# Performance work log

Measured on AMD Instinct MI355X. Metric: run time of the kernel, lower is better.

The kernel has to match this reference:

```python
import jax, jax.numpy as jnp
import numpy as np
from jax import lax

N = 128          # number of SDE time steps (== len(grad_u))
T_FINAL = 1.0    # t
D = 0.5          # diffusion coefficient
DT = T_FINAL / N
RB = 1.05        # assumed reflecting-sphere boundary radius for xb
B = 65536        # batch
H = 64           # FNN hidden width
SQRT2D = float(np.sqrt(2.0 * D))
# grad_eucl_polar buffer from the module
G_EP = jnp.array([[0.0, 0.0], [0.0, 1.0], [-1.0, 0.0]], dtype=jnp.float32)


def fnn(x, W0, b0, W1, b1, W2, b2):
    # utils.FNN(in,out,64,3): 3-layer tanh MLP
    h = jnp.tanh(x @ W0 + b0)
    h = jnp.tanh(h @ W1 + b1)
    return h @ W2 + b2


def t_inverse(a, phi):
    # T_inverse([theta - pi/2, phi]) = Rz(phi) @ Ry(a); maps fix_x=[1,0,0] to xt.
    ca, sa = jnp.cos(a), jnp.sin(a)
    cp, sp = jnp.cos(phi), jnp.sin(phi)
    z = jnp.zeros_like(a)
    r0 = jnp.stack([cp * ca, -sp, cp * sa], axis=-1)
    r1 = jnp.stack([sp * ca, cp, sp * sa], axis=-1)
    r2 = jnp.stack([-sa, z, ca], axis=-1)
    return jnp.stack([r0, r1, r2], axis=1)  # [B,3,3]


def _forward(xt0, dBt, W0u, b0u, W1u, b1u, W2u, b2u, Wg0, bg0, Wg1, bg1, Wg2, bg2):
    u_pre0 = fnn(xt0, W0u, b0u, W1u, b1u, W2u, b2u)  # u(x0), [B,1]
    eye = jnp.broadcast_to(jnp.eye(3, dtype=xt0.dtype), (xt0.shape[0], 3, 3))

    def step(carry, inp):
        xt, xt_in, gt, u_pre = carry
        dB, w0, c0, w1, c1, w2, c2 = inp
        # polar_corr(xt) with theta shifted by pi/2
        r = jnp.linalg.norm(xt, axis=1)
        theta = jnp.arccos(jnp.clip(xt[:, 2] / r, -0.999999, 0.999999))
        phi = jnp.arctan2(xt[:, 1], xt[:, 0])
        Ti = t_inverse(theta - jnp.pi / 2, phi)  # [B,3,3]
        # grad_u term: (g^T @ grad_trans @ T_inv)^T * grad_eucl_polar, summed over dim 1
        g = fnn(xt_in, w0, c0, w1, c1, w2, c2)  # [B,3]
        v = jnp.einsum('bi,bij,bjk->bk', g, gt, Ti)  # [B,3]
        gu = v @ G_EP  # [B,2]
        u_pre = u_pre + SQRT2D * jnp.sum(gu * dB, axis=1, keepdims=True)
        # sde_sphere step
        d = SQRT2D * dB
        td = d[:, 0] + jnp.pi / 2
        pd = d[:, 1]
        # transform_x(dXt) - fix_x  (spherical -> Cartesian, minus pole)
        dX3 = jnp.stack([jnp.sin(td) * jnp.cos(pd) - 1.0,
                         jnp.sin(td) * jnp.sin(pd),
                         jnp.cos(td)], axis=1)  # [B,3]
        dX = jnp.einsum('bij,bj->bi', Ti, dX3)
        xt = xt + dX
        xi = xt_in + jnp.einsum('bij,bj->bi', gt, dX)
        # go_back: reflect across sphere of radius RB where outside
        ri = jnp.linalg.norm(xi, axis=1)
        n = xi / ri[:, None]  # outward normal nb
        out = ri > RB
        xt_in = jnp.where(out[:, None], xi - 2.0 * (ri - RB)[:, None] * n, xi)
        # grad_trans += (-2 n n^T) grad_trans  where reflected (Householder)
        m = jnp.einsum('bj,bjk->bk', n, gt)
        gt = jnp.where(out[:, None, None], gt - 2.0 * n[:, :, None] * m[:, None, :], gt)
        return (xt, xt_in, gt, u_pre), None

    (xt, xt_in, gt, u_pre), _ = lax.scan(step, (xt0, xt0, eye, u_pre0),
                                         (dBt, Wg0, bg0, Wg1, bg1, Wg2, bg2))
    u_rel = jnp.sum(xt_in ** 2, axis=1, keepdims=True)  # assumed u0 terminal condition
    return u_pre, u_rel


def setup_inputs() -> dict:
    key = jax.random.key(0)
    ks = jax.random.split(key, 8)
    xt0 = jax.random.normal(ks[0], (B, 3), jnp.float32)
    xt0 = xt0 / jnp.linalg.norm(xt0, axis=1, keepdims=True)  # data_gen: points on unit sphere
    dBt = jax.random.normal(ks[1], (N, B, 2), jnp.float32) * np.float32(np.sqrt(DT))

    def w(k, shape, fan_in):
        return jax.random.normal(k, shape, jnp.float32) / np.float32(np.sqrt(fan_in))

    return {
        'xt0': xt0, 'dBt': dBt,
        'W0u': w(ks[2], (3, H), 3), 'b0u': jnp.zeros((H,), jnp.float32),
        'W1u': w(ks[3], (H, H), H), 'b1u': jnp.zeros((H,), jnp.float32),
        'W2u': w(ks[4], (H, 1), H), 'b2u': jnp.zeros((1,), jnp.float32),
        'Wg0': w(ks[5], (N, 3, H), 3), 'bg0': jnp.zeros((N, H), jnp.float32),
        'Wg1': w(ks[6], (N, H, H), H), 'bg1': jnp.zeros((N, H), jnp.float32),
        'Wg2': w(ks[7], (N, H, 3), H), 'bg2': jnp.zeros((N, 3), jnp.float32),
    }


def reference(xt0, dBt, W0u, b0u, W1u, b1u, W2u, b2u, Wg0, bg0, Wg1, bg1, Wg2, bg2):
    return _forward(xt0, dBt, W0u, b0u, W1u, b1u, W2u, b2u, Wg0, bg0, Wg1, bg1, Wg2, bg2)
```

## Files before the change

### kernel.cpp

```cpp
#include <hip/hip_runtime.h>

#define NB 65536
#define NSTEP 128
#define HD 64
#define RB 1.05f
#define SCALE 2.8853900817779268f
#define TBLK 928
#define OFF_A1 0
#define OFF_A0 512
#define OFF_A2 768
#define OFF_CB 896

typedef __bf16 bf16x8 __attribute__((ext_vector_type(8)));
typedef float f32x4 __attribute__((ext_vector_type(4)));
typedef unsigned int uint;
typedef unsigned short ushort;

extern "C" __device__ float __ocml_native_exp2_f32(float);
#if __has_builtin(__builtin_amdgcn_exp2f)
#define EXP2(x) __builtin_amdgcn_exp2f(x)
#else
#define EXP2(x) __ocml_native_exp2_f32(x)
#endif

__device__ __forceinline__ float tanh_fast(float x) {
    float e2 = __expf(2.0f * x);
    return 1.0f - 2.0f * __builtin_amdgcn_rcpf(1.0f + e2);
}

__device__ __forceinline__ void tanh2s(float za, float zb, float& ta, float& tb) {
    float ea = EXP2(za);
    float eb = EXP2(zb);
    float a1 = 1.0f + ea;
    float b1 = 1.0f + eb;
    float rp = __builtin_amdgcn_rcpf(a1 * b1);
    ta = fmaf(-2.0f * b1, rp, 1.0f);
    tb = fmaf(-2.0f * a1, rp, 1.0f);
}

__device__ __forceinline__ void sincos_small(float x, float& s, float& c) {
    float x2 = x * x;
    s = fmaf(x2, fmaf(x2, 8.3333333e-3f, -0.16666667f), 1.0f) * x;
    c = fmaf(x2, fmaf(x2, fmaf(x2, -1.3888889e-3f, 4.1666668e-2f), -0.5f), 1.0f);
}

__device__ __forceinline__ uint pack_bf16_trunc(float a, float b) {
    return __builtin_amdgcn_perm(__float_as_uint(b), __float_as_uint(a), 0x07060302u);
}

__device__ __forceinline__ ushort bf16_rne(float f) {
    uint u = __float_as_uint(f);
    u += 0x7fffu + ((u >> 16) & 1u);
    return (ushort)(u >> 16);
}


__global__ __launch_bounds__(256) void prep_a1(const float* __restrict__ Wg1,
                                               uint4* __restrict__ wsB) {
    int tid  = blockIdx.x * 256 + threadIdx.x;
    int lane = tid & 63;
    int I    = (tid >> 6) & 3;
    int kk   = (tid >> 8) & 1;
    int t    = tid >> 9;
    int rA   = lane & 15;
    int lrow = (I & 1) * 4 + (I >> 1) * 32 + (rA >> 2) * 8 + (rA & 3);
    int k0   = kk * 32 + ((lane >> 4) & 3) * 8;
    const float* src = Wg1 + ((size_t)t * HD + k0) * HD + lrow;
    ushort o[8];
#pragma unroll
    for (int e = 0; e < 8; e++) o[e] = bf16_rne(src[(size_t)e * HD] * SCALE);
    uint4 v;
    v.x = (uint)o[0] | ((uint)o[1] << 16);
    v.y = (uint)o[2] | ((uint)o[3] << 16);
    v.z = (uint)o[4] | ((uint)o[5] << 16);
    v.w = (uint)o[6] | ((uint)o[7] << 16);
    wsB[(size_t)t * TBLK + OFF_A1 + (kk * 4 + I) * 64 + lane] = v;
}

__global__ __launch_bounds__(256) void prep_a0(const float* __restrict__ Wg0,
                                               const float* __restrict__ bg0,
                                               uint4* __restrict__ wsB) {
    int tid  = blockIdx.x * 256 + threadIdx.x;
    int lane = tid & 63;
    int I    = (tid >> 6) & 3;
    int t    = tid >> 8;
    int m    = lane & 15;
    int kg   = (lane >> 4) & 3;
    int h    = (I >> 1) * 32 + (m >> 2) * 8 + (I & 1) * 4 + (m & 3);
    ushort o[8];
#pragma unroll
    for (int e = 0; e < 8; e++) {
        int k = kg * 8 + e;
        float v;
        if (k < 3)       v = SCALE * Wg0[((size_t)t * 3 + k) * HD + h];
        else if (k == 3) v = SCALE * bg0[(size_t)t * HD + h];
        else             v = 0.0f;
        o[e] = bf16_rne(v);
    }
    uint4 v;
    v.x = (uint)o[0] | ((uint)o[1] << 16);
    v.y = (uint)o[2] | ((uint)o[3] << 16);
    v.z = (uint)o[4] | ((uint)o[5] << 16);
    v.w = (uint)o[6] | ((uint)o[7] << 16);
    wsB[(size_t)t * TBLK + OFF_A0 + I * 64 + lane] = v;
}

__global__ __launch_bounds__(256) void prep_a2(const float* __restrict__ Wg2,
                                               uint4* __restrict__ wsB) {
    int tid  = blockIdx.x * 256 + threadIdx.x;
    int lane = tid & 63;
    int kk   = (tid >> 6) & 1;
    int t    = tid >> 7;
    int row  = lane & 15;
    int k0   = kk * 32 + ((lane >> 4) & 3) * 8;
    ushort o[8];
#pragma unroll
    for (int e = 0; e < 8; e++) {
        float v = (row < 3) ? Wg2[(size_t)t * HD * 3 + (size_t)(k0 + e) * 3 + row] : 0.0f;
        o[e] = bf16_rne(v);
    }
    uint4 v;
    v.x = (uint)o[0] | ((uint)o[1] << 16);
    v.y = (uint)o[2] | ((uint)o[3] << 16);
    v.z = (uint)o[4] | ((uint)o[5] << 16);
    v.w = (uint)o[6] | ((uint)o[7] << 16);
    wsB[(size_t)t * TBLK + OFF_A2 + kk * 64 + lane] = v;
}

__global__ __launch_bounds__(256) void prep_bias(const float* __restrict__ bg1,
                                                 uint4* __restrict__ wsB) {
    int tid = blockIdx.x * 256 + threadIdx.x;
    int i   = tid & 127;
    int t   = tid >> 7;
    int r   = i & 63;
    int pi  = ((r >> 4) & 1) * 4 + ((r >> 5) & 1) * 32 + ((r >> 2) & 3) * 8 + (r & 3);
    float* dst = (float*)(wsB + (size_t)t * TBLK + OFF_CB);
    dst[i] = (i < 64) ? (SCALE * bg1[(size_t)t * HD + pi]) : 0.0f;
}

__device__ __forceinline__ void mlp_h2_unpacked(float xx, float xy, float xz,
                                                const float* __restrict__ w0,
                                                const float* __restrict__ c0,
                                                const float* __restrict__ w1,
                                                int lane, f32x4* acc) {
    const int g16 = (lane >> 4) & 3;
    const int l15 = lane & 15;
#pragma unroll
    for (int kk = 0; kk < 2; kk++) {
        bf16x8 af[4];
#pragma unroll
        for (int I = 0; I < 4; I++) {
            uint pk[4];
#pragma unroll
            for (int ep = 0; ep < 4; ep++) {
                float f0 = w1[(kk * 32 + g16 * 8 + 2 * ep + 0) * HD + I * 16 + l15];
                float f1 = w1[(kk * 32 + g16 * 8 + 2 * ep + 1) * HD + I * 16 + l15];
                pk[ep] = (uint)bf16_rne(f0) | ((uint)bf16_rne(f1) << 16);
            }
            uint4 v; v.x = pk[0]; v.y = pk[1]; v.z = pk[2]; v.w = pk[3];
            af[I] = __builtin_bit_cast(bf16x8, v);
        }
        const float* wk = w0 + kk * 32 + g16 * 8;
        float4 wxa = *(const float4*)(wk);
        float4 wxb = *(const float4*)(wk + 4);
        float4 wya = *(const float4*)(wk + HD);
        float4 wyb = *(const float4*)(wk + HD + 4);
        float4 wza = *(const float4*)(wk + 2 * HD);
        float4 wzb = *(const float4*)(wk + 2 * HD + 4);
        const float* ck = c0 + kk * 32 + g16 * 8;
        float4 cva = *(const float4*)(ck);
        float4 cvb = *(const float4*)(ck + 4);
        float p0 = fmaf(xx, wxa.x, fmaf(xy, wya.x, fmaf(xz, wza.x, cva.x)));
        float p1 = fmaf(xx, wxa.y, fmaf(xy, wya.y, fmaf(xz, wza.y, cva.y)));
        float p2 = fmaf(xx, wxa.z, fmaf(xy, wya.z, fmaf(xz, wza.z, cva.z)));
        float p3 = fmaf(xx, wxa.w, fmaf(xy, wya.w, fmaf(xz, wza.w, cva.w)));
        float p4 = fmaf(xx, wxb.x, fmaf(xy, wyb.x, fmaf(xz, wzb.x, cvb.x)));
        float p5 = fmaf(xx, wxb.y, fmaf(xy, wyb.y, fmaf(xz, wzb.y, cvb.y)));
        float p6 = fmaf(xx, wxb.z, fmaf(xy, wyb.z, fmaf(xz, wzb.z, cvb.z)));
        float p7 = fmaf(xx, wxb.w, fmaf(xy, wyb.w, fmaf(xz, wzb.w, cvb.w)));
        uint4 bv;
        bv.x = pack_bf16_trunc(tanh_fast(p0), tanh_fast(p1));
        bv.y = pack_bf16_trunc(tanh_fast(p2), tanh_fast(p3));
        bv.z = pack_bf16_trunc(tanh_fast(p4), tanh_fast(p5));
        bv.w = pack_bf16_trunc(tanh_fast(p6), tanh_fast(p7));
        bf16x8 bf = __builtin_bit_cast(bf16x8, bv);
#pragma unroll
        for (int I = 0; I < 4; I++)
            acc[I] = __builtin_amdgcn_mfma_f32_16x16x32_bf16(af[I], bf, acc[I], 0, 0, 0);
    }
}

__global__ __launch_bounds__(256, 4) void sde_fast(
    const float* __restrict__ xt0,
    const float* __restrict__ dBt,
    const float* __restrict__ W0u, const float* __restrict__ b0u,
    const float* __restrict__ W1u, const float* __restrict__ b1u,
    const float* __restrict__ W2u, const float* __restrict__ b2u,
    const float* __restrict__ bg2,
    const uint4* __restrict__ wsB,
    float* __restrict__ out)
{
    const int tid  = threadIdx.x;
    const int lane = tid & 63;
    const int wv   = tid >> 6;
    const int g16  = (lane >> 4) & 3;
    const int l15  = lane & 15;
    const int p    = blockIdx.x * 64 + wv * 16 + l15;

    float xtx = xt0[p * 3 + 0];
    float xty = xt0[p * 3 + 1];
    float xtz = xt0[p * 3 + 2];
    float xix = xtx, xiy = xty, xiz = xtz;
    float g00 = 1.f, g01 = 0.f, g02 = 0.f;
    float g10 = 0.f, g11 = 1.f, g12 = 0.f;
    float g20 = 0.f, g21 = 0.f, g22 = 1.f;

    float u_pre;
    {
        f32x4 acc[4];
#pragma unroll
        for (int I = 0; I < 4; I++) acc[I] = (f32x4){0.f, 0.f, 0.f, 0.f};
        mlp_h2_unpacked(xtx, xty, xtz, W0u, b0u, W1u, lane, acc);
        float pj = 0.f;
#pragma unroll
        for (int I = 0; I < 4; I++) {
            float4 wv2 = *(const float4*)(W2u + I * 16 + g16 * 4);
            float4 cv  = *(const float4*)(b1u + I * 16 + g16 * 4);
            pj = fmaf(tanh_fast(acc[I][0] + cv.x), wv2.x, pj);
            pj = fmaf(tanh_fast(acc[I][1] + cv.y), wv2.y, pj);
            pj = fmaf(tanh_fast(acc[I][2] + cv.z), wv2.z, pj);
            pj = fmaf(tanh_fast(acc[I][3] + cv.w), wv2.w, pj);
        }
        pj += __shfl_xor(pj, 16, 64);
        pj += __shfl_xor(pj, 32, 64);
        u_pre = pj + b2u[0];
    }

    const f32x4 zero4 = (f32x4){0.f, 0.f, 0.f, 0.f};

#pragma unroll 1
    for (int t = 0; t < NSTEP; t++) {
        const uint4* blob_t = wsB + (size_t)t * TBLK;
        const float* c1p_t  = (const float*)(blob_t + OFF_CB);
        const float* c2     = bg2 + (size_t)t * 3;

        float d  = fmaf(xtx, xtx, fmaf(xty, xty, xtz * xtz));
        float rs = __builtin_amdgcn_rsqf(d);
        float uu = xtz * rs;
        uu = fminf(fmaxf(uu, -0.999999f), 0.999999f);
        float sa = -uu;
        float rho2 = fmaf(xtx, xtx, xty * xty);
        bool hasrho = rho2 > 0.0f;
        float rr = __builtin_amdgcn_rsqf(rho2);
        float cp = hasrho ? (xtx * rr) : 1.0f;
        float sp = hasrho ? (xty * rr) : 0.0f;
        float ca = hasrho ? (rho2 * rr * rs) : 1.4142135e-3f;
        float T00 = cp * ca, T01 = -sp, T02 = cp * sa;
        float T10 = sp * ca, T11 = cp,  T12 = sp * sa;
        float T20 = -sa,               T22 = ca;

        uint4 b0v;
        b0v.x = pack_bf16_trunc(xix, xiy);
        b0v.y = pack_bf16_trunc(xiz, 1.0f);
        b0v.z = 0u; b0v.w = 0u;
        bf16x8 b0 = __builtin_bit_cast(bf16x8, b0v);
        f32x4 acc0[4];
#pragma unroll
        for (int I = 0; I < 4; I++) {
            bf16x8 a0 = __builtin_bit_cast(bf16x8, blob_t[OFF_A0 + I * 64 + lane]);
            acc0[I] = __builtin_amdgcn_mfma_f32_16x16x32_bf16(a0, b0, zero4, 0, 0, 0);
        }

        f32x4 acc[4];
#pragma unroll
        for (int I = 0; I < 4; I++) {
            float4 cv = *(const float4*)(c1p_t + I * 16 + g16 * 4);
            acc[I] = (f32x4){cv.x, cv.y, cv.z, cv.w};
        }
#pragma unroll
        for (int kk = 0; kk < 2; kk++) {
            float t0, t1, t2, t3, t4, t5, t6, t7;
            tanh2s(acc0[kk * 2 + 0][0], acc0[kk * 2 + 0][1], t0, t1);
            tanh2s(acc0[kk * 2 + 0][2], acc0[kk * 2 + 0][3], t2, t3);
            tanh2s(acc0[kk * 2 + 1][0], acc0[kk * 2 + 1][1], t4, t5);
            tanh2s(acc0[kk * 2 + 1][2], acc0[kk * 2 + 1][3], t6, t7);
            uint4 bv;
            bv.x = pack_bf16_trunc(t0, t1);
            bv.y = pack_bf16_trunc(t2, t3);
            bv.z = pack_bf16_trunc(t4, t5);
            bv.w = pack_bf16_trunc(t6, t7);
            bf16x8 bf = __builtin_bit_cast(bf16x8, bv);
#pragma unroll
            for (int I = 0; I < 4; I++) {
                bf16x8 af = __builtin_bit_cast(bf16x8, blob_t[OFF_A1 + (kk * 4 + I) * 64 + lane]);
                acc[I] = __builtin_amdgcn_mfma_f32_16x16x32_bf16(af, bf, acc[I], 0, 0, 0);
            }
        }

        f32x4 acc2 = zero4;
#pragma unroll
        for (int half = 0; half < 2; half++) {
            float t0, t1, t2, t3, t4, t5, t6, t7;
            tanh2s(acc[2 * half + 0][0], acc[2 * half + 0][1], t0, t1);
            tanh2s(acc[2 * half + 0][2], acc[2 * half + 0][3], t2, t3);
            tanh2s(acc[2 * half + 1][0], acc[2 * half + 1][1], t4, t5);
            tanh2s(acc[2 * half + 1][2], acc[2 * half + 1][3], t6, t7);
            uint4 bv;
            bv.x = pack_bf16_trunc(t0, t1);
            bv.y = pack_bf16_trunc(t2, t3);
            bv.z = pack_bf16_trunc(t4, t5);
            bv.w = pack_bf16_trunc(t6, t7);
            bf16x8 bf = __builtin_bit_cast(bf16x8, bv);
            bf16x8 a2 = __builtin_bit_cast(bf16x8, blob_t[OFF_A2 + half * 64 + lane]);
            acc2 = __builtin_amdgcn_mfma_f32_16x16x32_bf16(a2, bf, acc2, 0, 0, 0);
        }
        float gv0 = __shfl(acc2[0], l15, 64) + c2[0];
        float gv1 = __shfl(acc2[1], l15, 64) + c2[1];
        float gv2 = __shfl(acc2[2], l15, 64) + c2[2];

        float M01 = fmaf(-sp, g00, cp * g01);
        float M11 = fmaf(-sp, g10, cp * g11);
        float M21 = fmaf(-sp, g20, cp * g21);
        float M02 = fmaf(g00, T02, fmaf(g01, T12, g02 * T22));
        float M12 = fmaf(g10, T02, fmaf(g11, T12, g12 * T22));
        float M22 = fmaf(g20, T02, fmaf(g21, T12, g22 * T22));
        float v1 = fmaf(gv0, M01, fmaf(gv1, M11, gv2 * M21));
        float v2 = fmaf(gv0, M02, fmaf(gv1, M12, gv2 * M22));

        const float2 dB = *(const float2*)(dBt + ((size_t)t * NB + p) * 2);
        float dB0 = dB.x, dB1 = dB.y;
        u_pre += fmaf(v1, dB1, -v2 * dB0);

        float s0d, c0d, s1d, c1d;
        sincos_small(dB0, s0d, c0d);
        sincos_small(dB1, s1d, c1d);
        float dx30 = fmaf(c0d, c1d, -1.0f);
        float dx31 = c0d * s1d;
        float dx32 = -s0d;

        float dX0 = fmaf(T00, dx30, fmaf(T01, dx31, T02 * dx32));
        float dX1 = fmaf(T10, dx30, fmaf(T11, dx31, T12 * dx32));
        float dX2 = fmaf(T20, dx30, T22 * dx32);

        xtx += dX0; xty += dX1; xtz += dX2;

        float xi0 = xix + fmaf(g00, dX0, fmaf(g01, dX1, g02 * dX2));
        float xi1 = xiy + fmaf(g10, dX0, fmaf(g11, dX1, g12 * dX2));
        float xi2 = xiz + fmaf(g20, dX0, fmaf(g21, dX1, g22 * dX2));

        float ri2 = fmaf(xi0, xi0, fmaf(xi1, xi1, xi2 * xi2));
        float rs2 = __builtin_amdgcn_rsqf(ri2);
        float ri  = ri2 * rs2;
        bool outb = ri > RB;
        float n0 = xi0 * rs2, n1 = xi1 * rs2, n2 = xi2 * rs2;
        float coefs = outb ? (2.0f * (ri - RB)) : 0.0f;

        xix = fmaf(-coefs, n0, xi0);
        xiy = fmaf(-coefs, n1, xi1);
        xiz = fmaf(-coefs, n2, xi2);

        float mm0 = fmaf(n0, g00, fmaf(n1, g10, n2 * g20));
        float mm1 = fmaf(n0, g01, fmaf(n1, g11, n2 * g21));
        float mm2 = fmaf(n0, g02, fmaf(n1, g12, n2 * g22));
        float tw  = outb ? 2.0f : 0.0f;
        float tn0 = tw * n0, tn1 = tw * n1, tn2 = tw * n2;
        g00 = fmaf(-tn0, mm0, g00);
        g01 = fmaf(-tn0, mm1, g01);
        g02 = fmaf(-tn0, mm2, g02);
        g10 = fmaf(-tn1, mm0, g10);
        g11 = fmaf(-tn1, mm1, g11);
        g12 = fmaf(-tn1, mm2, g12);
        g20 = fmaf(-tn2, mm0, g20);
        g21 = fmaf(-tn2, mm1, g21);
        g22 = fmaf(-tn2, mm2, g22);
    }

    float u_rel = fmaf(xix, xix, fmaf(xiy, xiy, xiz * xiz));
    if (g16 == 0) {
        out[p] = u_pre;
        out[NB + p] = u_rel;
    }
}

__global__ __launch_bounds__(256, 4) void sde_ref(
    const float* __restrict__ xt0,
    const float* __restrict__ dBt,
    const float* __restrict__ W0u, const float* __restrict__ b0u,
    const float* __restrict__ W1u, const float* __restrict__ b1u,
    const float* __restrict__ W2u, const float* __restrict__ b2u,
    const float* __restrict__ Wg0, const float* __restrict__ bg0,
    const float* __restrict__ Wg1, const float* __restrict__ bg1,
    const float* __restrict__ Wg2, const float* __restrict__ bg2,
    float* __restrict__ out)
{
    const int tid  = threadIdx.x;
    const int lane = tid & 63;
    const int wv   = tid >> 6;
    const int g16  = (lane >> 4) & 3;
    const int l15  = lane & 15;
    const int p    = blockIdx.x * 64 + wv * 16 + l15;

    float xtx = xt0[p * 3 + 0];
    float xty = xt0[p * 3 + 1];
    float xtz = xt0[p * 3 + 2];
    float xix = xtx, xiy = xty, xiz = xtz;
    float g00 = 1.f, g01 = 0.f, g02 = 0.f;
    float g10 = 0.f, g11 = 1.f, g12 = 0.f;
    float g20 = 0.f, g21 = 0.f, g22 = 1.f;

    float u_pre;
    {
        f32x4 acc[4];
#pragma unroll
        for (int I = 0; I < 4; I++) acc[I] = (f32x4){0.f, 0.f, 0.f, 0.f};
        mlp_h2_unpacked(xtx, xty, xtz, W0u, b0u, W1u, lane, acc);
        float pj = 0.f;
#pragma unroll
        for (int I = 0; I < 4; I++) {
            float4 wv2 = *(const float4*)(W2u + I * 16 + g16 * 4);
            float4 cv  = *(const float4*)(b1u + I * 16 + g16 * 4);
            pj = fmaf(tanh_fast(acc[I][0] + cv.x), wv2.x, pj);
            pj = fmaf(tanh_fast(acc[I][1] + cv.y), wv2.y, pj);
            pj = fmaf(tanh_fast(acc[I][2] + cv.z), wv2.z, pj);
            pj = fmaf(tanh_fast(acc[I][3] + cv.w), wv2.w, pj);
        }
        pj += __shfl_xor(pj, 16, 64);
        pj += __shfl_xor(pj, 32, 64);
        u_pre = pj + b2u[0];
    }

#pragma unroll 1
    for (int t = 0; t < NSTEP; t++) {
        const float* w0 = Wg0 + (size_t)t * 3 * HD;
        const float* c0 = bg0 + (size_t)t * HD;
        const float* c1 = bg1 + (size_t)t * HD;
        const float* w2 = Wg2 + (size_t)t * HD * 3;
        const float* c2 = bg2 + (size_t)t * 3;

        float r = sqrtf(fmaf(xtx, xtx, fmaf(xty, xty, xtz * xtz)));
        float uu = xtz / r;
        uu = fminf(fmaxf(uu, -0.999999f), 0.999999f);
        float ca = sqrtf((1.0f - uu) * (1.0f + uu));
        float sa = -uu;
        float rho = sqrtf(fmaf(xtx, xtx, xty * xty));
        float cp = (rho > 0.0f) ? (xtx / rho) : 1.0f;
        float sp = (rho > 0.0f) ? (xty / rho) : 0.0f;
        float T00 = cp * ca, T01 = -sp, T02 = cp * sa;
        float T10 = sp * ca, T11 = cp,  T12 = sp * sa;
        float T20 = -sa,               T22 = ca;

        f32x4 acc[4];
#pragma unroll
        for (int I = 0; I < 4; I++) acc[I] = (f32x4){0.f, 0.f, 0.f, 0.f};
        mlp_h2_unpacked(xix, xiy, xiz, w0, c0, Wg1 + (size_t)t * HD * HD, lane, acc);

        float pj0 = 0.f, pj1 = 0.f, pj2 = 0.f;
#pragma unroll
        for (int I = 0; I < 4; I++) {
            const float* wp = w2 + 3 * (I * 16 + g16 * 4);
            float4 wa = *(const float4*)(wp);
            float4 wb = *(const float4*)(wp + 4);
            float4 wc = *(const float4*)(wp + 8);
            float4 cv = *(const float4*)(c1 + I * 16 + g16 * 4);
            float th0 = tanh_fast(acc[I][0] + cv.x);
            float th1 = tanh_fast(acc[I][1] + cv.y);
            float th2 = tanh_fast(acc[I][2] + cv.z);
            float th3 = tanh_fast(acc[I][3] + cv.w);
            pj0 = fmaf(th0, wa.x, pj0); pj1 = fmaf(th0, wa.y, pj1); pj2 = fmaf(th0, wa.z, pj2);
            pj0 = fmaf(th1, wa.w, pj0); pj1 = fmaf(th1, wb.x, pj1); pj2 = fmaf(th1, wb.y, pj2);
            pj0 = fmaf(th2, wb.z, pj0); pj1 = fmaf(th2, wb.w, pj1); pj2 = fmaf(th2, wc.x, pj2);
            pj0 = fmaf(th3, wc.y, pj0); pj1 = fmaf(th3, wc.z, pj1); pj2 = fmaf(th3, wc.w, pj2);
        }
        pj0 += __shfl_xor(pj0, 16, 64); pj0 += __shfl_xor(pj0, 32, 64);
        pj1 += __shfl_xor(pj1, 16, 64); pj1 += __shfl_xor(pj1, 32, 64);
        pj2 += __shfl_xor(pj2, 16, 64); pj2 += __shfl_xor(pj2, 32, 64);
        float gv0 = pj0 + c2[0];
        float gv1 = pj1 + c2[1];
        float gv2 = pj2 + c2[2];

        float M01 = fmaf(-sp, g00, cp * g01);
        float M11 = fmaf(-sp, g10, cp * g11);
        float M21 = fmaf(-sp, g20, cp * g21);
        float M02 = fmaf(g00, T02, fmaf(g01, T12, g02 * T22));
        float M12 = fmaf(g10, T02, fmaf(g11, T12, g12 * T22));
        float M22 = fmaf(g20, T02, fmaf(g21, T12, g22 * T22));
        float v1 = fmaf(gv0, M01, fmaf(gv1, M11, gv2 * M21));
        float v2 = fmaf(gv0, M02, fmaf(gv1, M12, gv2 * M22));

        const float2 dB = *(const float2*)(dBt + ((size_t)t * NB + p) * 2);
        float dB0 = dB.x, dB1 = dB.y;
        u_pre += fmaf(v1, dB1, -v2 * dB0);

        float s0d, c0d, s1d, c1d;
        __sincosf(dB0, &s0d, &c0d);
        __sincosf(dB1, &s1d, &c1d);
        float dx30 = fmaf(c0d, c1d, -1.0f);
        float dx31 = c0d * s1d;
        float dx32 = -s0d;

        float dX0 = fmaf(T00, dx30, fmaf(T01, dx31, T02 * dx32));
        float dX1 = fmaf(T10, dx30, fmaf(T11, dx31, T12 * dx32));
        float dX2 = fmaf(T20, dx30, T22 * dx32);

        xtx += dX0; xty += dX1; xtz += dX2;

        float xi0 = xix + fmaf(g00, dX0, fmaf(g01, dX1, g02 * dX2));
        float xi1 = xiy + fmaf(g10, dX0, fmaf(g11, dX1, g12 * dX2));
        float xi2 = xiz + fmaf(g20, dX0, fmaf(g21, dX1, g22 * dX2));

        float ri = sqrtf(fmaf(xi0, xi0, fmaf(xi1, xi1, xi2 * xi2)));
        bool outb = ri > RB;
        float n0 = xi0 / ri, n1 = xi1 / ri, n2 = xi2 / ri;
        float coef = 2.0f * (ri - RB);

        xix = outb ? fmaf(-coef, n0, xi0) : xi0;
        xiy = outb ? fmaf(-coef, n1, xi1) : xi1;
        xiz = outb ? fmaf(-coef, n2, xi2) : xi2;

        float mm0 = fmaf(n0, g00, fmaf(n1, g10, n2 * g20));
        float mm1 = fmaf(n0, g01, fmaf(n1, g11, n2 * g21));
        float mm2 = fmaf(n0, g02, fmaf(n1, g12, n2 * g22));
        float tn0 = 2.0f * n0, tn1 = 2.0f * n1, tn2 = 2.0f * n2;
        g00 = outb ? fmaf(-tn0, mm0, g00) : g00;
        g01 = outb ? fmaf(-tn0, mm1, g01) : g01;
        g02 = outb ? fmaf(-tn0, mm2, g02) : g02;
        g10 = outb ? fmaf(-tn1, mm0, g10) : g10;
        g11 = outb ? fmaf(-tn1, mm1, g11) : g11;
        g12 = outb ? fmaf(-tn1, mm2, g12) : g12;
        g20 = outb ? fmaf(-tn2, mm0, g20) : g20;
        g21 = outb ? fmaf(-tn2, mm1, g21) : g21;
        g22 = outb ? fmaf(-tn2, mm2, g22) : g22;
    }

    float u_rel = fmaf(xix, xix, fmaf(xiy, xiy, xiz * xiz));
    if (g16 == 0) {
        out[p] = u_pre;
        out[NB + p] = u_rel;
    }
}

extern "C" void kernel_launch(void* const* d_in, const int* in_sizes, int n_in,
                              void* d_out, int out_size, void* d_ws, size_t ws_size,
                              hipStream_t stream) {
    const float* xt0 = (const float*)d_in[0];
    const float* dBt = (const float*)d_in[1];
    const float* W0u = (const float*)d_in[2];
    const float* b0u = (const float*)d_in[3];
    const float* W1u = (const float*)d_in[4];
    const float* b1u = (const float*)d_in[5];
    const float* W2u = (const float*)d_in[6];
    const float* b2u = (const float*)d_in[7];
    const float* Wg0 = (const float*)d_in[8];
    const float* bg0 = (const float*)d_in[9];
    const float* Wg1 = (const float*)d_in[10];
    const float* bg1 = (const float*)d_in[11];
    const float* Wg2 = (const float*)d_in[12];
    const float* bg2 = (const float*)d_in[13];
    float* out = (float*)d_out;

    const size_t needed = (size_t)NSTEP * TBLK * sizeof(uint4);
    dim3 grid(NB * 4 / 256), block(256);
    if (ws_size >= needed && d_ws != nullptr) {
        uint4* wsB = (uint4*)d_ws;
        hipLaunchKernelGGL(prep_a1,  dim3(256), dim3(256), 0, stream, Wg1, wsB);
        hipLaunchKernelGGL(prep_a0,  dim3(128), dim3(256), 0, stream, Wg0, bg0, wsB);
        hipLaunchKernelGGL(prep_a2,  dim3(64),  dim3(256), 0, stream, Wg2, wsB);
        hipLaunchKernelGGL(prep_bias, dim3(64), dim3(256), 0, stream, bg1, wsB);
        hipLaunchKernelGGL(sde_fast, grid, block, 0, stream,
                           xt0, dBt, W0u, b0u, W1u, b1u, W2u, b2u,
                           bg2, (const uint4*)wsB, out);
    } else {
        hipLaunchKernelGGL(sde_ref, grid, block, 0, stream,
                           xt0, dBt, W0u, b0u, W1u, b1u, W2u, b2u,
                           Wg0, bg0, Wg1, bg1, Wg2, bg2, out);
    }
}
```

Before: 415.9 us.

## Split SDE into state pass and time-parallel MLP pass with reduction

```diff
diff --git a/kernel.cpp b/kernel.cpp
--- a/kernel.cpp
+++ b/kernel.cpp
@@ -56,16 +56,19 @@
 
 
 __global__ __launch_bounds__(256) void prep_a1(const float* __restrict__ Wg1,
+                                               const float* __restrict__ W1u,
                                                uint4* __restrict__ wsB) {
     int tid  = blockIdx.x * 256 + threadIdx.x;
     int lane = tid & 63;
     int I    = (tid >> 6) & 3;
     int kk   = (tid >> 8) & 1;
     int t    = tid >> 9;
+    if (t > NSTEP) return;
     int rA   = lane & 15;
     int lrow = (I & 1) * 4 + (I >> 1) * 32 + (rA >> 2) * 8 + (rA & 3);
     int k0   = kk * 32 + ((lane >> 4) & 3) * 8;
-    const float* src = Wg1 + ((size_t)t * HD + k0) * HD + lrow;
+    const float* base = (t < NSTEP) ? (Wg1 + (size_t)t * HD * HD) : W1u;
+    const float* src  = base + (size_t)k0 * HD + lrow;
     ushort o[8];
 #pragma unroll
     for (int e = 0; e < 8; e++) o[e] = bf16_rne(src[(size_t)e * HD] * SCALE);
@@ -79,11 +82,14 @@
 
 __global__ __launch_bounds__(256) void prep_a0(const float* __restrict__ Wg0,
                                                const float* __restrict__ bg0,
+                                               const float* __restrict__ W0u,
+                                               const float* __restrict__ b0u,
                                                uint4* __restrict__ wsB) {
     int tid  = blockIdx.x * 256 + threadIdx.x;
     int lane = tid & 63;
     int I    = (tid >> 6) & 3;
     int t    = tid >> 8;
+    if (t > NSTEP) return;
     int m    = lane & 15;
     int kg   = (lane >> 4) & 3;
     int h    = (I >> 1) * 32 + (m >> 2) * 8 + (I & 1) * 4 + (m & 3);
@@ -91,10 +97,10 @@
 #pragma unroll
     for (int e = 0; e < 8; e++) {
         int k = kg * 8 + e;
-        float v;
-        if (k < 3)       v = SCALE * Wg0[((size_t)t * 3 + k) * HD + h];
-        else if (k == 3) v = SCALE * bg0[(size_t)t * HD + h];
-        else             v = 0.0f;
+        float v = 0.0f;
+        if (k < 3)       v = SCALE * ((t < NSTEP) ? Wg0[((size_t)t * 3 + k) * HD + h]
+                                                  : W0u[(size_t)k * HD + h]);
+        else if (k == 3) v = SCALE * ((t < NSTEP) ? bg0[(size_t)t * HD + h] : b0u[h]);
         o[e] = bf16_rne(v);
     }
     uint4 v;
@@ -106,17 +112,24 @@
 }
 
 __global__ __launch_bounds__(256) void prep_a2(const float* __restrict__ Wg2,
+                                               const float* __restrict__ W2u,
                                                uint4* __restrict__ wsB) {
     int tid  = blockIdx.x * 256 + threadIdx.x;
     int lane = tid & 63;
     int kk   = (tid >> 6) & 1;
     int t    = tid >> 7;
+    if (t > NSTEP) return;
     int row  = lane & 15;
+    int j    = row & 3;
     int k0   = kk * 32 + ((lane >> 4) & 3) * 8;
     ushort o[8];
 #pragma unroll
     for (int e = 0; e < 8; e++) {
-        float v = (row < 3) ? Wg2[(size_t)t * HD * 3 + (size_t)(k0 + e) * 3 + row] : 0.0f;
+        float v = 0.0f;
+        if (j < 3) {
+            if (t < NSTEP) v = Wg2[(size_t)t * HD * 3 + (size_t)(k0 + e) * 3 + j];
+            else           v = (j == 0) ? W2u[k0 + e] : 0.0f;
+        }
         o[e] = bf16_rne(v);
     }
     uint4 v;
@@ -128,14 +141,234 @@
 }
 
 __global__ __launch_bounds__(256) void prep_bias(const float* __restrict__ bg1,
+                                                 const float* __restrict__ b1u,
                                                  uint4* __restrict__ wsB) {
     int tid = blockIdx.x * 256 + threadIdx.x;
     int i   = tid & 127;
     int t   = tid >> 7;
+    if (t > NSTEP) return;
     int r   = i & 63;
     int pi  = ((r >> 4) & 1) * 4 + ((r >> 5) & 1) * 32 + ((r >> 2) & 3) * 8 + (r & 3);
     float* dst = (float*)(wsB + (size_t)t * TBLK + OFF_CB);
-    dst[i] = (i < 64) ? (SCALE * bg1[(size_t)t * HD + pi]) : 0.0f;
+    float v = 0.0f;
+    if (i < 64) v = SCALE * ((t < NSTEP) ? bg1[(size_t)t * HD + pi] : b1u[pi]);
+    dst[i] = v;
+}
+
+__device__ __forceinline__ f32x4 mlp_chain(float xx, float xy, float xz,
+                                           const uint4* __restrict__ blob_t,
+                                           int lane, int g16) {
+    const f32x4 zero4 = (f32x4){0.f, 0.f, 0.f, 0.f};
+    uint4 b0v;
+    b0v.x = pack_bf16_trunc(xx, xy);
+    b0v.y = pack_bf16_trunc(xz, 1.0f);
+    b0v.z = 0u; b0v.w = 0u;
+    bf16x8 b0 = __builtin_bit_cast(bf16x8, b0v);
+
+    uint4 a0v0 = {0u,0u,0u,0u}, a0v1 = {0u,0u,0u,0u}, a0v2 = {0u,0u,0u,0u}, a0v3 = {0u,0u,0u,0u};
+    if (g16 == 0) {
+        a0v0 = blob_t[OFF_A0 + 0 * 64 + lane];
+        a0v1 = blob_t[OFF_A0 + 1 * 64 + lane];
+        a0v2 = blob_t[OFF_A0 + 2 * 64 + lane];
+        a0v3 = blob_t[OFF_A0 + 3 * 64 + lane];
+    }
+    f32x4 acc0[4];
+    acc0[0] = __builtin_amdgcn_mfma_f32_16x16x32_bf16(__builtin_bit_cast(bf16x8, a0v0), b0, zero4, 0, 0, 0);
+    acc0[1] = __builtin_amdgcn_mfma_f32_16x16x32_bf16(__builtin_bit_cast(bf16x8, a0v1), b0, zero4, 0, 0, 0);
+    acc0[2] = __builtin_amdgcn_mfma_f32_16x16x32_bf16(__builtin_bit_cast(bf16x8, a0v2), b0, zero4, 0, 0, 0);
+    acc0[3] = __builtin_amdgcn_mfma_f32_16x16x32_bf16(__builtin_bit_cast(bf16x8, a0v3), b0, zero4, 0, 0, 0);
+
+    const float* c1p_t = (const float*)(blob_t + OFF_CB);
+    f32x4 acc[4];
+#pragma unroll
+    for (int I = 0; I < 4; I++) {
+        float4 cv = *(const float4*)(c1p_t + I * 16 + g16 * 4);
+        acc[I] = (f32x4){cv.x, cv.y, cv.z, cv.w};
+    }
+#pragma unroll
+    for (int kk = 0; kk < 2; kk++) {
+        float t0, t1, t2, t3, t4, t5, t6, t7;
+        tanh2s(acc0[kk * 2 + 0][0], acc0[kk * 2 + 0][1], t0, t1);
+        tanh2s(acc0[kk * 2 + 0][2], acc0[kk * 2 + 0][3], t2, t3);
+        tanh2s(acc0[kk * 2 + 1][0], acc0[kk * 2 + 1][1], t4, t5);
+        tanh2s(acc0[kk * 2 + 1][2], acc0[kk * 2 + 1][3], t6, t7);
+        uint4 bv;
+        bv.x = pack_bf16_trunc(t0, t1);
+        bv.y = pack_bf16_trunc(t2, t3);
+        bv.z = pack_bf16_trunc(t4, t5);
+        bv.w = pack_bf16_trunc(t6, t7);
+        bf16x8 bf = __builtin_bit_cast(bf16x8, bv);
+#pragma unroll
+        for (int I = 0; I < 4; I++) {
+            bf16x8 af = __builtin_bit_cast(bf16x8, blob_t[OFF_A1 + (kk * 4 + I) * 64 + lane]);
+            acc[I] = __builtin_amdgcn_mfma_f32_16x16x32_bf16(af, bf, acc[I], 0, 0, 0);
+        }
+    }
+    f32x4 acc2 = zero4;
+#pragma unroll
+    for (int half = 0; half < 2; half++) {
+        float t0, t1, t2, t3, t4, t5, t6, t7;
+        tanh2s(acc[2 * half + 0][0], acc[2 * half + 0][1], t0, t1);
+        tanh2s(acc[2 * half + 0][2], acc[2 * half + 0][3], t2, t3);
+        tanh2s(acc[2 * half + 1][0], acc[2 * half + 1][1], t4, t5);
+        tanh2s(acc[2 * half + 1][2], acc[2 * half + 1][3], t6, t7);
+        uint4 bv;
+        bv.x = pack_bf16_trunc(t0, t1);
+        bv.y = pack_bf16_trunc(t2, t3);
+        bv.z = pack_bf16_trunc(t4, t5);
+        bv.w = pack_bf16_trunc(t6, t7);
+        bf16x8 bf = __builtin_bit_cast(bf16x8, bv);
+        bf16x8 a2 = __builtin_bit_cast(bf16x8, blob_t[OFF_A2 + half * 64 + lane]);
+        acc2 = __builtin_amdgcn_mfma_f32_16x16x32_bf16(a2, bf, acc2, 0, 0, 0);
+    }
+    return acc2;
+}
+
+__global__ __launch_bounds__(256) void sde_state(
+    const float* __restrict__ xt0, const float* __restrict__ dBt,
+    float4* __restrict__ xiw4, float2* __restrict__ w2f,
+    float* __restrict__ out)
+{
+    int p = blockIdx.x * 256 + threadIdx.x;
+    float xtx = xt0[p * 3 + 0];
+    float xty = xt0[p * 3 + 1];
+    float xtz = xt0[p * 3 + 2];
+    float xix = xtx, xiy = xty, xiz = xtz;
+    float g00 = 1.f, g01 = 0.f, g02 = 0.f;
+    float g10 = 0.f, g11 = 1.f, g12 = 0.f;
+    float g20 = 0.f, g21 = 0.f, g22 = 1.f;
+
+    float2 dBa = *(const float2*)(dBt + (size_t)p * 2);
+    float2 dBb = *(const float2*)(dBt + ((size_t)NB + p) * 2);
+
+#pragma unroll 1
+    for (int t = 0; t < NSTEP; t++) {
+        float d  = fmaf(xtx, xtx, fmaf(xty, xty, xtz * xtz));
+        float rs = __builtin_amdgcn_rsqf(d);
+        float uu = xtz * rs;
+        uu = fminf(fmaxf(uu, -0.999999f), 0.999999f);
+        float sa = -uu;
+        float rho2 = fmaf(xtx, xtx, xty * xty);
+        bool hasrho = rho2 > 0.0f;
+        float rr = __builtin_amdgcn_rsqf(rho2);
+        float cp = hasrho ? (xtx * rr) : 1.0f;
+        float sp = hasrho ? (xty * rr) : 0.0f;
+        float ca = hasrho ? (rho2 * rr * rs) : 1.4142135e-3f;
+        float T00 = cp * ca, T01 = -sp, T02 = cp * sa;
+        float T10 = sp * ca, T11 = cp,  T12 = sp * sa;
+        float T20 = -sa,               T22 = ca;
+
+        float M01 = fmaf(-sp, g00, cp * g01);
+        float M11 = fmaf(-sp, g10, cp * g11);
+        float M21 = fmaf(-sp, g20, cp * g21);
+        float M02 = fmaf(g00, T02, fmaf(g01, T12, g02 * T22));
+        float M12 = fmaf(g10, T02, fmaf(g11, T12, g12 * T22));
+        float M22 = fmaf(g20, T02, fmaf(g21, T12, g22 * T22));
+
+        float dB0 = dBa.x, dB1 = dBa.y;
+        float w0 = fmaf(dB1, M01, -(dB0 * M02));
+        float w1 = fmaf(dB1, M11, -(dB0 * M12));
+        float w2v = fmaf(dB1, M21, -(dB0 * M22));
+
+        xiw4[(size_t)t * NB + p] = make_float4(xix, xiy, xiz, w0);
+        w2f[(size_t)t * NB + p]  = make_float2(w1, w2v);
+
+        float s0d, c0d, s1d, c1d;
+        sincos_small(dB0, s0d, c0d);
+        sincos_small(dB1, s1d, c1d);
+        float dx30 = fmaf(c0d, c1d, -1.0f);
+        float dx31 = c0d * s1d;
+        float dx32 = -s0d;
+
+        float dX0 = fmaf(T00, dx30, fmaf(T01, dx31, T02 * dx32));
+        float dX1 = fmaf(T10, dx30, fmaf(T11, dx31, T12 * dx32));
+        float dX2 = fmaf(T20, dx30, T22 * dx32);
+
+        xtx += dX0; xty += dX1; xtz += dX2;
+
+        float xi0 = xix + fmaf(g00, dX0, fmaf(g01, dX1, g02 * dX2));
+        float xi1 = xiy + fmaf(g10, dX0, fmaf(g11, dX1, g12 * dX2));
+        float xi2 = xiz + fmaf(g20, dX0, fmaf(g21, dX1, g22 * dX2));
+
+        float ri2 = fmaf(xi0, xi0, fmaf(xi1, xi1, xi2 * xi2));
+        float rs2 = __builtin_amdgcn_rsqf(ri2);
+        float ri  = ri2 * rs2;
+        bool outb = ri > RB;
+        float n0 = xi0 * rs2, n1 = xi1 * rs2, n2 = xi2 * rs2;
+        float coefs = outb ? (2.0f * (ri - RB)) : 0.0f;
+
+        xix = fmaf(-coefs, n0, xi0);
+        xiy = fmaf(-coefs, n1, xi1);
+        xiz = fmaf(-coefs, n2, xi2);
+
+        float mm0 = fmaf(n0, g00, fmaf(n1, g10, n2 * g20));
+        float mm1 = fmaf(n0, g01, fmaf(n1, g11, n2 * g21));
+        float mm2 = fmaf(n0, g02, fmaf(n1, g12, n2 * g22));
+        float tw  = outb ? 2.0f : 0.0f;
+        float tn0 = tw * n0, tn1 = tw * n1, tn2 = tw * n2;
+        g00 = fmaf(-tn0, mm0, g00);
+        g01 = fmaf(-tn0, mm1, g01);
+        g02 = fmaf(-tn0, mm2, g02);
+        g10 = fmaf(-tn1, mm0, g10);
+        g11 = fmaf(-tn1, mm1, g11);
+        g12 = fmaf(-tn1, mm2, g12);
+        g20 = fmaf(-tn2, mm0, g20);
+        g21 = fmaf(-tn2, mm1, g21);
+        g22 = fmaf(-tn2, mm2, g22);
+
+        dBa = dBb;
+        int tn = (t + 2 < NSTEP) ? (t + 2) : (NSTEP - 1);
+        dBb = *(const float2*)(dBt + ((size_t)tn * NB + p) * 2);
+    }
+    out[NB + p] = fmaf(xix, xix, fmaf(xiy, xiy, xiz * xiz));
+}
+
+__global__ __launch_bounds__(256, 6) void sde_mlp(
+    const float* __restrict__ xt0,
+    const float4* __restrict__ xiw4, const float2* __restrict__ w2f,
+    const uint4* __restrict__ wsB,
+    const float* __restrict__ bg2, const float* __restrict__ b2u,
+    float* __restrict__ partial)
+{
+    const int tid  = threadIdx.x;
+    const int lane = tid & 63;
+    const int wv   = tid >> 6;
+    const int g16  = (lane >> 4) & 3;
+    const int l15  = lane & 15;
+    const int blk  = blockIdx.x;
+    const int chunk = blk >> 10;
+    const int p    = (blk & 1023) * 64 + wv * 16 + l15;
+
+    float u_loc = 0.0f;
+    if (chunk == 0) {
+        float xx = xt0[p * 3 + 0];
+        float xy = xt0[p * 3 + 1];
+        float xz = xt0[p * 3 + 2];
+        f32x4 a2 = mlp_chain(xx, xy, xz, wsB + (size_t)NSTEP * TBLK, lane, g16);
+        u_loc = a2[0] + b2u[0];
+    }
+
+#pragma unroll 1
+    for (int s = 0; s < 16; s++) {
+        int t = chunk * 16 + s;
+        float4 xw  = xiw4[(size_t)t * NB + p];
+        float2 w12 = w2f[(size_t)t * NB + p];
+        f32x4 a2 = mlp_chain(xw.x, xw.y, xw.z, wsB + (size_t)t * TBLK, lane, g16);
+        const float* c2 = bg2 + (size_t)t * 3;
+        u_loc = fmaf(a2[0] + c2[0], xw.w,  u_loc);
+        u_loc = fmaf(a2[1] + c2[1], w12.x, u_loc);
+        u_loc = fmaf(a2[2] + c2[2], w12.y, u_loc);
+    }
+    if (g16 == 0) partial[(size_t)chunk * NB + p] = u_loc;
+}
+
+__global__ __launch_bounds__(256) void sde_reduce(const float* __restrict__ partial,
+                                                  float* __restrict__ out) {
+    int p = blockIdx.x * 256 + threadIdx.x;
+    float s = 0.0f;
+#pragma unroll
+    for (int c = 0; c < 8; c++) s += partial[(size_t)c * NB + p];
+    out[p] = s;
 }
 
 __device__ __forceinline__ void mlp_h2_unpacked(float xx, float xy, float xz,
@@ -236,12 +469,9 @@
         u_pre = pj + b2u[0];
     }
 
-    const f32x4 zero4 = (f32x4){0.f, 0.f, 0.f, 0.f};
-
 #pragma unroll 1
     for (int t = 0; t < NSTEP; t++) {
         const uint4* blob_t = wsB + (size_t)t * TBLK;
-        const float* c1p_t  = (const float*)(blob_t + OFF_CB);
         const float* c2     = bg2 + (size_t)t * 3;
 
         float d  = fmaf(xtx, xtx, fmaf(xty, xty, xtz * xtz));
@@ -259,64 +489,10 @@
         float T10 = sp * ca, T11 = cp,  T12 = sp * sa;
         float T20 = -sa,               T22 = ca;
 
-        uint4 b0v;
-        b0v.x = pack_bf16_trunc(xix, xiy);
-        b0v.y = pack_bf16_trunc(xiz, 1.0f);
-        b0v.z = 0u; b0v.w = 0u;
-        bf16x8 b0 = __builtin_bit_cast(bf16x8, b0v);
-        f32x4 acc0[4];
-#pragma unroll
-        for (int I = 0; I < 4; I++) {
-            bf16x8 a0 = __builtin_bit_cast(bf16x8, blob_t[OFF_A0 + I * 64 + lane]);
-            acc0[I] = __builtin_amdgcn_mfma_f32_16x16x32_bf16(a0, b0, zero4, 0, 0, 0);
-        }
-
-        f32x4 acc[4];
-#pragma unroll
-        for (int I = 0; I < 4; I++) {
-            float4 cv = *(const float4*)(c1p_t + I * 16 + g16 * 4);
-            acc[I] = (f32x4){cv.x, cv.y, cv.z, cv.w};
-        }
-#pragma unroll
-        for (int kk = 0; kk < 2; kk++) {
-            float t0, t1, t2, t3, t4, t5, t6, t7;
-            tanh2s(acc0[kk * 2 + 0][0], acc0[kk * 2 + 0][1], t0, t1);
-            tanh2s(acc0[kk * 2 + 0][2], acc0[kk * 2 + 0][3], t2, t3);
-            tanh2s(acc0[kk * 2 + 1][0], acc0[kk * 2 + 1][1], t4, t5);
-            tanh2s(acc0[kk * 2 + 1][2], acc0[kk * 2 + 1][3], t6, t7);
-            uint4 bv;
-            bv.x = pack_bf16_trunc(t0, t1);
-            bv.y = pack_bf16_trunc(t2, t3);
-            bv.z = pack_bf16_trunc(t4, t5);
-            bv.w = pack_bf16_trunc(t6, t7);
-            bf16x8 bf = __builtin_bit_cast(bf16x8, bv);
-#pragma unroll
-            for (int I = 0; I < 4; I++) {
-                bf16x8 af = __builtin_bit_cast(bf16x8, blob_t[OFF_A1 + (kk * 4 + I) * 64 + lane]);
-                acc[I] = __builtin_amdgcn_mfma_f32_16x16x32_bf16(af, bf, acc[I], 0, 0, 0);
-            }
-        }
-
-        f32x4 acc2 = zero4;
-#pragma unroll
-        for (int half = 0; half < 2; half++) {
-            float t0, t1, t2, t3, t4, t5, t6, t7;
-            tanh2s(acc[2 * half + 0][0], acc[2 * half + 0][1], t0, t1);
-            tanh2s(acc[2 * half + 0][2], acc[2 * half + 0][3], t2, t3);
-            tanh2s(acc[2 * half + 1][0], acc[2 * half + 1][1], t4, t5);
-            tanh2s(acc[2 * half + 1][2], acc[2 * half + 1][3], t6, t7);
-            uint4 bv;
-            bv.x = pack_bf16_trunc(t0, t1);
-            bv.y = pack_bf16_trunc(t2, t3);
-            bv.z = pack_bf16_trunc(t4, t5);
-            bv.w = pack_bf16_trunc(t6, t7);
-            bf16x8 bf = __builtin_bit_cast(bf16x8, bv);
-            bf16x8 a2 = __builtin_bit_cast(bf16x8, blob_t[OFF_A2 + half * 64 + lane]);
-            acc2 = __builtin_amdgcn_mfma_f32_16x16x32_bf16(a2, bf, acc2, 0, 0, 0);
-        }
-        float gv0 = __shfl(acc2[0], l15, 64) + c2[0];
-        float gv1 = __shfl(acc2[1], l15, 64) + c2[1];
-        float gv2 = __shfl(acc2[2], l15, 64) + c2[2];
+        f32x4 a2 = mlp_chain(xix, xiy, xiz, blob_t, lane, g16);
+        float gv0 = a2[0] + c2[0];
+        float gv1 = a2[1] + c2[1];
+        float gv2 = a2[2] + c2[2];
 
         float M01 = fmaf(-sp, g00, cp * g01);
         float M11 = fmaf(-sp, g10, cp * g11);
@@ -558,19 +734,38 @@
     const float* bg2 = (const float*)d_in[13];
     float* out = (float*)d_out;
 
-    const size_t needed = (size_t)NSTEP * TBLK * sizeof(uint4);
-    dim3 grid(NB * 4 / 256), block(256);
-    if (ws_size >= needed && d_ws != nullptr) {
+    const size_t SZ_BLOB = (size_t)(NSTEP + 1) * TBLK * sizeof(uint4);
+    const size_t SZ_XIW  = (size_t)NSTEP * NB * sizeof(float4);
+    const size_t SZ_W2   = (size_t)NSTEP * NB * sizeof(float2);
+    const size_t SZ_PART = (size_t)8 * NB * sizeof(float);
+
+    if (ws_size >= SZ_BLOB + SZ_XIW + SZ_W2 + SZ_PART && d_ws != nullptr) {
+        uint4*  wsB     = (uint4*)d_ws;
+        float4* xiw4    = (float4*)((char*)d_ws + SZ_BLOB);
+        float2* w2f     = (float2*)((char*)d_ws + SZ_BLOB + SZ_XIW);
+        float*  partial = (float*)((char*)d_ws + SZ_BLOB + SZ_XIW + SZ_W2);
+        hipLaunchKernelGGL(prep_a1,  dim3(258), dim3(256), 0, stream, Wg1, W1u, wsB);
+        hipLaunchKernelGGL(prep_a0,  dim3(129), dim3(256), 0, stream, Wg0, bg0, W0u, b0u, wsB);
+        hipLaunchKernelGGL(prep_a2,  dim3(65),  dim3(256), 0, stream, Wg2, W2u, wsB);
+        hipLaunchKernelGGL(prep_bias, dim3(65), dim3(256), 0, stream, bg1, b1u, wsB);
+        hipLaunchKernelGGL(sde_state, dim3(NB / 256), dim3(256), 0, stream,
+                           xt0, dBt, xiw4, w2f, out);
+        hipLaunchKernelGGL(sde_mlp, dim3(8192), dim3(256), 0, stream,
+                           xt0, (const float4*)xiw4, (const float2*)w2f,
+                           (const uint4*)wsB, bg2, b2u, partial);
+        hipLaunchKernelGGL(sde_reduce, dim3(NB / 256), dim3(256), 0, stream,
+                           (const float*)partial, out);
+    } else if (ws_size >= SZ_BLOB && d_ws != nullptr) {
         uint4* wsB = (uint4*)d_ws;
-        hipLaunchKernelGGL(prep_a1,  dim3(256), dim3(256), 0, stream, Wg1, wsB);
-        hipLaunchKernelGGL(prep_a0,  dim3(128), dim3(256), 0, stream, Wg0, bg0, wsB);
-        hipLaunchKernelGGL(prep_a2,  dim3(64),  dim3(256), 0, stream, Wg2, wsB);
-        hipLaunchKernelGGL(prep_bias, dim3(64), dim3(256), 0, stream, bg1, wsB);
-        hipLaunchKernelGGL(sde_fast, grid, block, 0, stream,
+        hipLaunchKernelGGL(prep_a1,  dim3(258), dim3(256), 0, stream, Wg1, W1u, wsB);
+        hipLaunchKernelGGL(prep_a0,  dim3(129), dim3(256), 0, stream, Wg0, bg0, W0u, b0u, wsB);
+        hipLaunchKernelGGL(prep_a2,  dim3(65),  dim3(256), 0, stream, Wg2, W2u, wsB);
+        hipLaunchKernelGGL(prep_bias, dim3(65), dim3(256), 0, stream, bg1, b1u, wsB);
+        hipLaunchKernelGGL(sde_fast, dim3(NB * 4 / 256), dim3(256), 0, stream,
                            xt0, dBt, W0u, b0u, W1u, b1u, W2u, b2u,
                            bg2, (const uint4*)wsB, out);
     } else {
-        hipLaunchKernelGGL(sde_ref, grid, block, 0, stream,
+        hipLaunchKernelGGL(sde_ref, dim3(NB * 4 / 256), dim3(256), 0, stream,
                            xt0, dBt, W0u, b0u, W1u, b1u, W2u, b2u,
                            Wg0, bg0, Wg1, bg1, Wg2, bg2, out);
     }
```

Result: faster. 385.1 us (-7.4%).
